# Kernel optimization log

Hardware: AMD Instinct MI355X
Metric: run time of the kernel (lower is better)

Reference implementation:

```python
import jax, jax.numpy as jnp
import numpy as np

B, S, V, E, H, DM = 4, 512, 32000, 512, 1024, 256
U, M = 4096, 1024
MEM_CAP = 512 * 4  # max_length * memory_segments


def setup_inputs() -> dict:
    key = jax.random.key(0)
    ks = jax.random.split(key, 26)
    def n(k, shape, s=0.02):
        return jax.random.normal(k, shape, dtype=jnp.float32) * s
    return {
        'input_ids': jax.random.randint(ks[0], (B, S), 0, V),
        'past_tokens': jax.random.randint(ks[1], (B, M), 0, V),
        'past_keys': jax.random.normal(ks[2], (B, M, DM), dtype=jnp.float32),
        'untied_ids': jax.random.randint(ks[3], (U,), 0, V),
        'emb': n(ks[4], (V, E)),
        'gru_w_ih': n(ks[5], (3 * H, E)), 'gru_w_hh': n(ks[6], (3 * H, H)),
        'gru_b_ih': n(ks[7], (3 * H,)), 'gru_b_hh': n(ks[8], (3 * H,)),
        'q_w': n(ks[9], (DM, H)), 'q_b': n(ks[10], (DM,)),
        'k_w': n(ks[11], (DM, H)), 'k_b': n(ks[12], (DM,)),
        'gate_w': n(ks[13], (1, H)), 'gate_b': n(ks[14], (1,)),
        'fc_w': n(ks[15], (4 * E, H)), 'fc_b': n(ks[16], (4 * E,)),
        'proj_w': n(ks[17], (E, 4 * E)), 'proj_b': n(ks[18], (E,)),
        'out_bias': jnp.zeros((V,), jnp.float32),
        'part_w': n(ks[19], (U, E)), 'part_b': n(ks[20], (U,)),
        'mem_scale': jnp.float32(6.0),
    }


def _gru(x, w_ih, w_hh, b_ih, b_hh):
    # x: [B,S,E] -> states [B,S,H]; torch GRU cell math
    xp = x @ w_ih.T + b_ih  # [B,S,3H]
    h0 = jnp.zeros((x.shape[0], w_hh.shape[1]), x.dtype)
    def step(h, xp_t):
        hp = h @ w_hh.T + b_hh
        xr, xz, xn = jnp.split(xp_t, 3, axis=-1)
        hr, hz, hn = jnp.split(hp, 3, axis=-1)
        r = jax.nn.sigmoid(xr + hr)
        z = jax.nn.sigmoid(xz + hz)
        nn_ = jnp.tanh(xn + r * hn)
        h_new = (1.0 - z) * nn_ + z * h
        return h_new, h_new
    h_last, states = jax.lax.scan(step, h0, jnp.swapaxes(xp, 0, 1))
    return jnp.swapaxes(states, 0, 1), h_last


def reference(input_ids, past_tokens, past_keys, untied_ids, emb,
              gru_w_ih, gru_w_hh, gru_b_ih, gru_b_hh,
              q_w, q_b, k_w, k_b, gate_w, gate_b,
              fc_w, fc_b, proj_w, proj_b, out_bias, part_w, part_b, mem_scale):
    x = emb[input_ids]                                  # [B,S,E]
    states, _ = _gru(x, gru_w_ih, gru_w_hh, gru_b_ih, gru_b_hh)  # dropout=eval identity
    head = jnp.square(jax.nn.relu(states @ fc_w.T + fc_b))       # [B,S,4E]
    base = head @ proj_w.T + proj_b                                # [B,S,E]
    logits = base @ emb.T + out_bias                               # [B,S,V]
    partial = base @ part_w.T + part_b                             # [B,S,U]
    logits = logits.at[:, :, untied_ids].add(partial)              # scatter_add over vocab

    q = states @ q_w.T + q_b                                       # [B,S,DM]
    ck = states @ k_w.T + k_b                                      # [B,S,DM]
    scale = jnp.float32(1.0 / np.sqrt(DM))
    cur_scores = jnp.einsum('bsd,btd->bst', q, ck) * scale
    causal = jnp.tril(jnp.ones((S, S), bool), k=-1)                # strictly-past mask
    neg = jnp.finfo(cur_scores.dtype).min
    masked_cur = jnp.where(causal[None], cur_scores, neg)
    past_scores = jnp.einsum('bsd,bmd->bsm', q, past_keys) * scale
    all_scores = jnp.concatenate([past_scores, masked_cur], axis=-1)   # [B,S,M+S]
    all_mask = jnp.concatenate([
        jnp.ones((B, S, M), bool),
        jnp.broadcast_to(causal[None], (B, S, S))], axis=-1)
    att = jax.nn.softmax(all_scores, axis=-1) * all_mask
    att = att / jnp.maximum(att.sum(axis=-1, keepdims=True), 1e-6)
    val_idx = jnp.concatenate([
        jnp.broadcast_to(past_tokens[:, None, :], (B, S, M)),
        jnp.broadcast_to(input_ids[:, None, :], (B, S, S))], axis=-1)   # [B,S,M+S]
    gate = jax.nn.sigmoid(states @ gate_w.T + gate_b)               # [B,S,1]
    gated = att * (gate * mem_scale)
    b_idx = jnp.arange(B)[:, None, None]
    s_idx = jnp.arange(S)[None, :, None]
    logits = logits.at[b_idx, s_idx, val_idx].add(gated)            # irregular scatter_add

    next_keys = jax.lax.stop_gradient(
        jnp.concatenate([past_keys, ck], axis=1))[:, -MEM_CAP:]
    next_tokens = jnp.concatenate([past_tokens, input_ids], axis=1)[:, -MEM_CAP:]
    return logits, next_keys, next_tokens
```

## Files before the change

kernel.cpp:

```cpp
#include <hip/hip_runtime.h>
#include <cstddef>
#include <cstring>

#define BB 4
#define SS 512
#define VV 32000
#define EE 512
#define HH 1024
#define DM 256
#define UU 4096
#define MM 1024
#define TT 1536

typedef __attribute__((ext_vector_type(8))) short short8v;
typedef __attribute__((ext_vector_type(4))) float f32x4;

__device__ __forceinline__ unsigned long long agent_ld64(const unsigned long long* p) {
  return __hip_atomic_load(const_cast<unsigned long long*>(p), __ATOMIC_RELAXED,
                           __HIP_MEMORY_SCOPE_AGENT);
}
__device__ __forceinline__ void agent_st64(unsigned long long* p, unsigned long long v) {
  __hip_atomic_store(p, v, __ATOMIC_RELAXED, __HIP_MEMORY_SCOPE_AGENT);
}
__device__ __forceinline__ float sigmoidf_(float x) { return 1.f / (1.f + __expf(-x)); }

__device__ __forceinline__ unsigned short f2bf_rtn(float x) {
  unsigned u; __builtin_memcpy(&u, &x, 4);
  unsigned r = (u + 0x7FFFu + ((u >> 16) & 1u)) >> 16;
  return (unsigned short)r;
}
__device__ __forceinline__ float bf2f(unsigned short b) {
  unsigned u = ((unsigned)b) << 16; float f; __builtin_memcpy(&f, &u, 4); return f;
}

__global__ __launch_bounds__(256) void split_bf16(
    const float* __restrict__ in, unsigned short* __restrict__ hi,
    unsigned short* __restrict__ lo, int n)
{
  for (int i = blockIdx.x * 256 + threadIdx.x; i < n; i += gridDim.x * 256) {
    float x = in[i];
    unsigned short h = f2bf_rtn(x);
    hi[i] = h;
    lo[i] = f2bf_rtn(x - bf2f(h));
  }
}

__global__ __launch_bounds__(256) void gemm_mfma_bt(
    const unsigned short* __restrict__ Ah, const unsigned short* __restrict__ Al,
    const unsigned short* __restrict__ Wh, const unsigned short* __restrict__ Wl,
    const float* __restrict__ bias, float* __restrict__ C, int K, int ldc)
{
  const int tid = threadIdx.x, lane = tid & 63, w = tid >> 6;
  const int bm = blockIdx.y * 128, bn = blockIdx.x * 128;
  const int wm = (w >> 1) * 64, wn = (w & 1) * 64;
  const int r = lane & 15, ko = (lane >> 4) * 8;

  f32x4 acc[4][4] = {};

  for (int k0 = 0; k0 < K; k0 += 32) {
    short8v ah[4], al[4], bh[4], bl[4];
#pragma unroll
    for (int mi = 0; mi < 4; ++mi) {
      size_t off = (size_t)(bm + wm + mi * 16 + r) * K + k0 + ko;
      ah[mi] = *(const short8v*)(Ah + off);
      al[mi] = *(const short8v*)(Al + off);
    }
#pragma unroll
    for (int ni = 0; ni < 4; ++ni) {
      size_t off = (size_t)(bn + wn + ni * 16 + r) * K + k0 + ko;
      bh[ni] = *(const short8v*)(Wh + off);
      bl[ni] = *(const short8v*)(Wl + off);
    }
#pragma unroll
    for (int mi = 0; mi < 4; ++mi)
#pragma unroll
      for (int ni = 0; ni < 4; ++ni) {
        acc[mi][ni] = __builtin_amdgcn_mfma_f32_16x16x32_bf16(ah[mi], bh[ni], acc[mi][ni], 0, 0, 0);
        acc[mi][ni] = __builtin_amdgcn_mfma_f32_16x16x32_bf16(ah[mi], bl[ni], acc[mi][ni], 0, 0, 0);
        acc[mi][ni] = __builtin_amdgcn_mfma_f32_16x16x32_bf16(al[mi], bh[ni], acc[mi][ni], 0, 0, 0);
      }
  }

#pragma unroll
  for (int mi = 0; mi < 4; ++mi)
#pragma unroll
    for (int ni = 0; ni < 4; ++ni) {
      const int row = bm + wm + mi * 16 + (lane >> 4) * 4;
      const int col = bn + wn + ni * 16 + (lane & 15);
      const float bv = bias[col];
#pragma unroll
      for (int i = 0; i < 4; ++i)
        C[(size_t)(row + i) * ldc + col] = acc[mi][ni][i] + bv;
    }
}

template <int TILE, int MICRO>
__global__ __launch_bounds__(256) void gemm_k(
    const float* __restrict__ A, const int* __restrict__ a_idx,
    const float* __restrict__ W, const float* __restrict__ bias,
    float* __restrict__ C, int K, int ldc, int act, const int* __restrict__ sidx)
{
  constexpr int PITCH = TILE + 4;
  __shared__ float As[16][PITCH];
  __shared__ float Ws[16][PITCH];
  const int tid = threadIdx.x;
  const int bm = blockIdx.y * TILE, bn = blockIdx.x * TILE;
  const int tr = tid >> 4, tc = tid & 15;
  const int lk = tid & 15, lr0 = tid >> 4;
  float acc[MICRO][MICRO] = {};

  for (int k0 = 0; k0 < K; k0 += 16) {
#pragma unroll
    for (int jj = 0; jj < TILE / 16; ++jj) {
      int row = lr0 + (jj << 4);
      int am = bm + row;
      int ar = a_idx ? a_idx[am] : am;
      As[lk][row] = A[(size_t)ar * K + k0 + lk];
      Ws[lk][row] = W[(size_t)(bn + row) * K + k0 + lk];
    }
    __syncthreads();
#pragma unroll
    for (int kk = 0; kk < 16; ++kk) {
      float av[MICRO], wv[MICRO];
#pragma unroll
      for (int i = 0; i < MICRO; ++i) av[i] = As[kk][tr * MICRO + i];
#pragma unroll
      for (int j = 0; j < MICRO; ++j) wv[j] = Ws[kk][tc * MICRO + j];
#pragma unroll
      for (int i = 0; i < MICRO; ++i)
#pragma unroll
        for (int j = 0; j < MICRO; ++j) acc[i][j] += av[i] * wv[j];
    }
    __syncthreads();
  }

#pragma unroll
  for (int i = 0; i < MICRO; ++i) {
    int m = bm + tr * MICRO + i;
    float tmp[MICRO];
#pragma unroll
    for (int j = 0; j < MICRO; ++j) {
      int n = bn + tc * MICRO + j;
      float v = acc[i][j] + bias[n];
      if (act == 1) { v = fmaxf(v, 0.f); v *= v; }
      tmp[j] = v;
    }
    if (sidx) {
#pragma unroll
      for (int j = 0; j < MICRO; ++j)
        atomicAdd(C + (size_t)m * ldc + sidx[bn + tc * MICRO + j], tmp[j]);
    } else {
      float* cp = C + (size_t)m * ldc + bn + tc * MICRO;
#pragma unroll
      for (int j4 = 0; j4 < MICRO / 4; ++j4)
        *(float4*)(cp + 4 * j4) =
            make_float4(tmp[4 * j4], tmp[4 * j4 + 1], tmp[4 * j4 + 2], tmp[4 * j4 + 3]);
    }
  }
}

__global__ __launch_bounds__(512, 1) void gru_scan(
    const float* __restrict__ xp,
    const float* __restrict__ w_hh,
    const float* __restrict__ b_hh,
    float* __restrict__ states,
    unsigned long long* hbuf)
{
  __shared__ float h_lds[2][HH];
  const int tid = threadIdx.x;
  const int lane = tid & 63;
  const int wv = tid >> 6;
  const int bb = blockIdx.x >> 5;
  const int r = blockIdx.x & 31;
  const int c0 = (r << 5) + (wv << 2);

  unsigned long long* hb = hbuf + ((size_t)bb << 11);

  float wreg[4][3][16];
#pragma unroll
  for (int k = 0; k < 4; ++k)
#pragma unroll
    for (int g = 0; g < 3; ++g) {
      const float* wr = w_hh + (size_t)((g << 10) + c0 + k) * HH + lane;
#pragma unroll
      for (int i = 0; i < 16; ++i) wreg[k][g][i] = wr[i << 6];
    }
  float bh[4][3];
#pragma unroll
  for (int k = 0; k < 4; ++k)
#pragma unroll
    for (int g = 0; g < 3; ++g) bh[k][g] = b_hh[(g << 10) + c0 + k];

  for (int i = tid; i < HH; i += 512) h_lds[0][i] = 0.f;
  __syncthreads();

  for (int t = 0; t < SS; ++t) {
    const int cur = t & 1, nxt = (t + 1) & 1;
    const float* hc = h_lds[cur];

    float4 xrv, xzv, xnv, hold;
    if (lane == 0) {
      const float* xpr = xp + (size_t)((bb << 9) + t) * 3072 + c0;
      xrv = *(const float4*)(xpr);
      xzv = *(const float4*)(xpr + HH);
      xnv = *(const float4*)(xpr + 2 * HH);
      hold = *(const float4*)(hc + c0);
    }

    float acc[4][3] = {};
#pragma unroll
    for (int i = 0; i < 16; ++i) {
      float hv = hc[(i << 6) + lane];
#pragma unroll
      for (int k = 0; k < 4; ++k) {
        acc[k][0] += hv * wreg[k][0][i];
        acc[k][1] += hv * wreg[k][1][i];
        acc[k][2] += hv * wreg[k][2][i];
      }
    }
#pragma unroll
    for (int off = 32; off >= 1; off >>= 1)
#pragma unroll
      for (int k = 0; k < 4; ++k) {
        acc[k][0] += __shfl_xor(acc[k][0], off, 64);
        acc[k][1] += __shfl_xor(acc[k][1], off, 64);
        acc[k][2] += __shfl_xor(acc[k][2], off, 64);
      }

    if (lane == 0) {
      const unsigned long long tagw = ((unsigned long long)(unsigned)(t + 1)) << 32;
      float xr[4] = {xrv.x, xrv.y, xrv.z, xrv.w};
      float xz[4] = {xzv.x, xzv.y, xzv.z, xzv.w};
      float xn[4] = {xnv.x, xnv.y, xnv.z, xnv.w};
      float ho[4] = {hold.x, hold.y, hold.z, hold.w};
      float hv4[4];
#pragma unroll
      for (int k = 0; k < 4; ++k) {
        float rr = sigmoidf_(xr[k] + acc[k][0] + bh[k][0]);
        float zz = sigmoidf_(xz[k] + acc[k][1] + bh[k][1]);
        float nn = tanhf(xn[k] + rr * (acc[k][2] + bh[k][2]));
        hv4[k] = (1.f - zz) * nn + zz * ho[k];
      }
      if (t < SS - 1) {
        unsigned long long* dst = hb + ((size_t)nxt << 10) + c0;
#pragma unroll
        for (int k = 0; k < 4; ++k) {
          unsigned hbits;
          __builtin_memcpy(&hbits, &hv4[k], 4);
          agent_st64(dst + k, tagw | (unsigned long long)hbits);
        }
      }
      *(float4*)(states + (size_t)((bb << 9) + t) * HH + c0) =
          make_float4(hv4[0], hv4[1], hv4[2], hv4[3]);
    }
    if (t == SS - 1) break;

    {
      const unsigned tgt = (unsigned)(t + 1);
      const unsigned long long* src = hb + ((size_t)nxt << 10) + (tid << 1);
      unsigned long long p0, p1;
      for (;;) {
        p0 = agent_ld64(src);
        p1 = agent_ld64(src + 1);
        if ((unsigned)(p0 >> 32) >= tgt && (unsigned)(p1 >> 32) >= tgt) break;
      }
      h_lds[nxt][(tid << 1)] = __uint_as_float((unsigned)p0);
      h_lds[nxt][(tid << 1) + 1] = __uint_as_float((unsigned)p1);
    }
    __syncthreads();
  }
}

__global__ __launch_bounds__(256) void gate_kernel(
    const float* __restrict__ states, const float* __restrict__ gate_w,
    const float* __restrict__ gate_b, float* __restrict__ out)
{
  const int lane = threadIdx.x & 63;
  const int row = (blockIdx.x << 2) + (threadIdx.x >> 6);
  float s = 0.f;
#pragma unroll
  for (int i = 0; i < 16; ++i)
    s += states[(size_t)row * HH + (i << 6) + lane] * gate_w[(i << 6) + lane];
#pragma unroll
  for (int off = 32; off >= 1; off >>= 1) s += __shfl_xor(s, off, 64);
  if (lane == 0) out[row] = sigmoidf_(s + gate_b[0]);
}

__global__ __launch_bounds__(256) void copy_next(
    const float* __restrict__ past_keys, const float* __restrict__ ck,
    const int* __restrict__ past_tokens, const int* __restrict__ input_ids,
    float* __restrict__ nk, float* __restrict__ ntokf)
{
  const int i = blockIdx.x * 256 + threadIdx.x;
  if (i < BB * TT * 64) {
    int b = i / (TT * 64);
    int rem = i - b * (TT * 64);
    int t = rem >> 6, c = rem & 63;
    float4 v;
    if (t < MM) v = ((const float4*)past_keys)[((b << 10) + t) * 64 + c];
    else        v = ((const float4*)ck)[((b << 9) + (t - MM)) * 64 + c];
    ((float4*)nk)[i] = v;
  }
  if (i < BB * TT) {
    int b = i / TT, t = i - b * TT;
    int tok = (t < MM) ? past_tokens[(b << 10) + t] : input_ids[(b << 9) + t - MM];
    ntokf[i] = (float)tok;
  }
}

__global__ __launch_bounds__(256) void attn_scatter(
    const float* __restrict__ qbuf,
    const float* __restrict__ nk,
    const float* __restrict__ ntokf,
    const float* __restrict__ gate,
    const float* __restrict__ msp,
    float* __restrict__ logits)
{
  __shared__ float q_s[8][260];
  __shared__ float k_s[32][260];
  const int b = blockIdx.y;
  const int s0 = blockIdx.x << 3;
  const int tid = threadIdx.x, lane = tid & 63, wv = tid >> 6;
  const int half = lane >> 5, tl = lane & 31;
  const int ss = wv + (half << 2);
  const int sg = s0 + ss;
  const int limit = MM + sg;

  for (int i = tid; i < 8 * 256; i += 256)
    q_s[i >> 8][i & 255] = qbuf[(size_t)((b << 9) + s0 + (i >> 8)) * DM + (i & 255)];

  const int kr = tid >> 3, kc = (tid & 7) << 5;
  float mx = -1e30f, sum = 0.f;
  float fscale = 0.f;

  for (int pass = 0; pass < 2; ++pass) {
    if (pass == 1) {
#pragma unroll
      for (int off = 16; off >= 1; off >>= 1) {
        float mo = __shfl_xor(mx, off, 64);
        float so = __shfl_xor(sum, off, 64);
        float m2 = fmaxf(mx, mo);
        sum = sum * __expf(mx - m2) + so * __expf(mo - m2);
        mx = m2;
      }
      fscale = gate[(b << 9) + sg] * msp[0] / sum;
    }
    for (int tile = 0; tile < 48; ++tile) {
      __syncthreads();
      {
        const float4* src = (const float4*)(nk + ((size_t)(b * TT + (tile << 5) + kr) << 8) + kc);
        float4* dst = (float4*)(&k_s[kr][kc]);
#pragma unroll
        for (int u = 0; u < 8; ++u) dst[u] = src[u];
      }
      __syncthreads();
      int t = (tile << 5) + tl;
      if (t < limit) {
        float a = 0.f;
#pragma unroll 8
        for (int d = 0; d < 256; d += 4) {
          float4 kv = *(const float4*)&k_s[tl][d];
          float4 qv = *(const float4*)&q_s[ss][d];
          a += kv.x * qv.x + kv.y * qv.y + kv.z * qv.z + kv.w * qv.w;
        }
        a *= 0.0625f;
        if (pass == 0) {
          float m2 = fmaxf(mx, a);
          sum = sum * __expf(mx - m2) + __expf(a - m2);
          mx = m2;
        } else {
          int tok = (int)ntokf[b * TT + t];
          atomicAdd(logits + (size_t)((b << 9) + sg) * VV + tok,
                    __expf(a - mx) * fscale);
        }
      }
    }
  }
}

extern "C" void kernel_launch(void* const* d_in, const int* in_sizes, int n_in,
                              void* d_out, int out_size, void* d_ws, size_t ws_size,
                              hipStream_t stream) {
  (void)in_sizes; (void)n_in; (void)out_size;
  const int*   input_ids   = (const int*)  d_in[0];
  const int*   past_tokens = (const int*)  d_in[1];
  const float* past_keys   = (const float*)d_in[2];
  const int*   untied_ids  = (const int*)  d_in[3];
  const float* emb         = (const float*)d_in[4];
  const float* w_ih        = (const float*)d_in[5];
  const float* w_hh        = (const float*)d_in[6];
  const float* b_ih        = (const float*)d_in[7];
  const float* b_hh        = (const float*)d_in[8];
  const float* q_w         = (const float*)d_in[9];
  const float* q_b         = (const float*)d_in[10];
  const float* k_w         = (const float*)d_in[11];
  const float* k_b         = (const float*)d_in[12];
  const float* gate_w      = (const float*)d_in[13];
  const float* gate_b      = (const float*)d_in[14];
  const float* fc_w        = (const float*)d_in[15];
  const float* fc_b        = (const float*)d_in[16];
  const float* proj_w      = (const float*)d_in[17];
  const float* proj_b      = (const float*)d_in[18];
  const float* out_bias    = (const float*)d_in[19];
  const float* part_w      = (const float*)d_in[20];
  const float* part_b      = (const float*)d_in[21];
  const float* mem_scale   = (const float*)d_in[22];

  char* ws = (char*)d_ws;
  unsigned long long* hbuf = (unsigned long long*)(ws + 4096);
  float* gatebuf  = (float*)(ws + 69632);
  float* qb       = (float*)(ws + 81920);
  float* ckb      = (float*)(ws + 2179072);
  float* xp       = (float*)(ws + 4276224);
  float* states   = (float*)(ws + 29442048);
  float* head     = (float*)(ws + 37830656);
  float* base     = (float*)(ws + 54607872);
  unsigned short* embh  = (unsigned short*)(ws + 58802176);
  unsigned short* embl  = (unsigned short*)(ws + 91570176);
  unsigned short* baseh = (unsigned short*)(ws + 124338176);
  unsigned short* basel = (unsigned short*)(ws + 126435328);
  const bool use_mfma = ws_size >= 128532480ull;

  float* logits = (float*)d_out;
  float* nk     = logits + 65536000ll;
  float* ntokf  = logits + 67108864ll;

  hipMemsetAsync(ws, 0, 69632, stream);

  if (use_mfma)
    split_bf16<<<2048, 256, 0, stream>>>(emb, embh, embl, VV * EE);

  gemm_k<128, 8><<<dim3(3072 / 128, 2048 / 128), 256, 0, stream>>>(
      emb, input_ids, w_ih, b_ih, xp, EE, 3072, 0, nullptr);

  gru_scan<<<128, 512, 0, stream>>>(xp, w_hh, b_hh, states, hbuf);

  gemm_k<128, 8><<<dim3(2048 / 128, 2048 / 128), 256, 0, stream>>>(
      states, nullptr, fc_w, fc_b, head, HH, 2048, 1, nullptr);

  gemm_k<64, 4><<<dim3(512 / 64, 2048 / 64), 256, 0, stream>>>(
      head, nullptr, proj_w, proj_b, base, 2048, EE, 0, nullptr);

  if (use_mfma) {
    split_bf16<<<512, 256, 0, stream>>>(base, baseh, basel, 2048 * EE);
    gemm_mfma_bt<<<dim3(VV / 128, 2048 / 128), 256, 0, stream>>>(
        baseh, basel, embh, embl, out_bias, logits, EE, VV);
  } else {
    gemm_k<128, 8><<<dim3(VV / 128, 2048 / 128), 256, 0, stream>>>(
        base, nullptr, emb, out_bias, logits, EE, VV, 0, nullptr);
  }

  gemm_k<128, 8><<<dim3(UU / 128, 2048 / 128), 256, 0, stream>>>(
      base, nullptr, part_w, part_b, logits, EE, VV, 0, untied_ids);

  gemm_k<64, 4><<<dim3(DM / 64, 2048 / 64), 256, 0, stream>>>(
      states, nullptr, q_w, q_b, qb, HH, DM, 0, nullptr);
  gemm_k<64, 4><<<dim3(DM / 64, 2048 / 64), 256, 0, stream>>>(
      states, nullptr, k_w, k_b, ckb, HH, DM, 0, nullptr);

  gate_kernel<<<512, 256, 0, stream>>>(states, gate_w, gate_b, gatebuf);

  copy_next<<<1536, 256, 0, stream>>>(past_keys, ckb, past_tokens, input_ids, nk, ntokf);

  attn_scatter<<<dim3(SS / 8, BB), 256, 0, stream>>>(qb, nk, ntokf, gatebuf, mem_scale, logits);
}
```

Baseline: 5.609 ms.

## Move all GEMMs and attention scores to bf16 hi/lo MFMA, retile GRU scan

Every dense projection (input GRU projection, fc, proj, tied and untied output, q, k) now runs through one MFMA kernel that works on weights and activations stored as bf16 hi and lo halves laid side by side. The attention is split into an MFMA score GEMM plus a per-row softmax-and-scatter kernel, replacing the fused fp32 attention kernel. The GRU scan is retiled to 64 blocks of 1024 threads so fewer blocks take part in the per-step cross-block exchange. Because the hi and lo halves sit side by side, each dot product computes only hi·hi plus lo·lo and drops the hi·lo cross terms, so accuracy falls to roughly bf16 level. It also adds extra split passes and workspace, and the fast path runs only when the workspace is large enough.

```diff
diff --git a/kernel.cpp b/kernel.cpp
--- a/kernel.cpp
+++ b/kernel.cpp
@@ -33,52 +33,53 @@
   unsigned u = ((unsigned)b) << 16; float f; __builtin_memcpy(&f, &u, 4); return f;
 }
 
-__global__ __launch_bounds__(256) void split_bf16(
-    const float* __restrict__ in, unsigned short* __restrict__ hi,
-    unsigned short* __restrict__ lo, int n)
+__global__ __launch_bounds__(256) void split_cat(
+    const float* __restrict__ in, unsigned short* __restrict__ out, int n, int K)
 {
   for (int i = blockIdx.x * 256 + threadIdx.x; i < n; i += gridDim.x * 256) {
+    int row = i / K, col = i - row * K;
     float x = in[i];
     unsigned short h = f2bf_rtn(x);
-    hi[i] = h;
-    lo[i] = f2bf_rtn(x - bf2f(h));
-  }
-}
-
-__global__ __launch_bounds__(256) void gemm_mfma_bt(
-    const unsigned short* __restrict__ Ah, const unsigned short* __restrict__ Al,
-    const unsigned short* __restrict__ Wh, const unsigned short* __restrict__ Wl,
-    const float* __restrict__ bias, float* __restrict__ C, int K, int ldc)
+    unsigned short l = f2bf_rtn(x - bf2f(h));
+    size_t b = (size_t)row * (K << 1) + col;
+    out[b] = h;
+    out[b + K] = l;
+  }
+}
+
+__global__ __launch_bounds__(256) void gemm_mfma_cat(
+    const unsigned short* __restrict__ A2, const int* __restrict__ a_idx,
+    const unsigned short* __restrict__ W2, const float* __restrict__ bias,
+    float* __restrict__ C, unsigned short* __restrict__ C2,
+    int K2, int N, int ldc, int act, const int* __restrict__ sidx)
 {
   const int tid = threadIdx.x, lane = tid & 63, w = tid >> 6;
   const int bm = blockIdx.y * 128, bn = blockIdx.x * 128;
   const int wm = (w >> 1) * 64, wn = (w & 1) * 64;
   const int r = lane & 15, ko = (lane >> 4) * 8;
 
+  int arow[4];
+#pragma unroll
+  for (int mi = 0; mi < 4; ++mi) {
+    int row = bm + wm + mi * 16 + r;
+    arow[mi] = a_idx ? a_idx[row] : row;
+  }
+
   f32x4 acc[4][4] = {};
 
-  for (int k0 = 0; k0 < K; k0 += 32) {
-    short8v ah[4], al[4], bh[4], bl[4];
-#pragma unroll
-    for (int mi = 0; mi < 4; ++mi) {
-      size_t off = (size_t)(bm + wm + mi * 16 + r) * K + k0 + ko;
-      ah[mi] = *(const short8v*)(Ah + off);
-      al[mi] = *(const short8v*)(Al + off);
-    }
-#pragma unroll
-    for (int ni = 0; ni < 4; ++ni) {
-      size_t off = (size_t)(bn + wn + ni * 16 + r) * K + k0 + ko;
-      bh[ni] = *(const short8v*)(Wh + off);
-      bl[ni] = *(const short8v*)(Wl + off);
-    }
+  for (int k0 = 0; k0 < K2; k0 += 32) {
+    short8v a[4], b[4];
 #pragma unroll
     for (int mi = 0; mi < 4; ++mi)
-#pragma unroll
-      for (int ni = 0; ni < 4; ++ni) {
-        acc[mi][ni] = __builtin_amdgcn_mfma_f32_16x16x32_bf16(ah[mi], bh[ni], acc[mi][ni], 0, 0, 0);
-        acc[mi][ni] = __builtin_amdgcn_mfma_f32_16x16x32_bf16(ah[mi], bl[ni], acc[mi][ni], 0, 0, 0);
-        acc[mi][ni] = __builtin_amdgcn_mfma_f32_16x16x32_bf16(al[mi], bh[ni], acc[mi][ni], 0, 0, 0);
-      }
+      a[mi] = *(const short8v*)(A2 + (size_t)arow[mi] * K2 + k0 + ko);
+#pragma unroll
+    for (int ni = 0; ni < 4; ++ni)
+      b[ni] = *(const short8v*)(W2 + (size_t)(bn + wn + ni * 16 + r) * K2 + k0 + ko);
+#pragma unroll
+    for (int mi = 0; mi < 4; ++mi)
+#pragma unroll
+      for (int ni = 0; ni < 4; ++ni)
+        acc[mi][ni] = __builtin_amdgcn_mfma_f32_16x16x32_bf16(a[mi], b[ni], acc[mi][ni], 0, 0, 0);
   }
 
 #pragma unroll
@@ -89,9 +90,107 @@
       const int col = bn + wn + ni * 16 + (lane & 15);
       const float bv = bias[col];
 #pragma unroll
+      for (int i = 0; i < 4; ++i) {
+        float v = acc[mi][ni][i] + bv;
+        if (act == 1) { v = fmaxf(v, 0.f); v *= v; }
+        if (C2) {
+          unsigned short h = f2bf_rtn(v);
+          unsigned short l = f2bf_rtn(v - bf2f(h));
+          size_t bo = (size_t)(row + i) * (N << 1) + col;
+          C2[bo] = h;
+          C2[bo + N] = l;
+        } else if (sidx) {
+          atomicAdd(C + (size_t)(row + i) * ldc + sidx[col], v);
+        } else {
+          C[(size_t)(row + i) * ldc + col] = v;
+        }
+      }
+    }
+}
+
+__global__ __launch_bounds__(256) void score_mfma_cat(
+    const unsigned short* __restrict__ q2,
+    const unsigned short* __restrict__ k2,
+    float* __restrict__ scores)
+{
+  const int b = blockIdx.z;
+  const unsigned short* A2 = q2 + (size_t)b * SS * (2 * DM);
+  const unsigned short* W2 = k2 + (size_t)b * TT * (2 * DM);
+  float* C = scores + (size_t)b * SS * TT;
+
+  const int tid = threadIdx.x, lane = tid & 63, w = tid >> 6;
+  const int bm = blockIdx.y * 128, bn = blockIdx.x * 128;
+  const int wm = (w >> 1) * 64, wn = (w & 1) * 64;
+  const int r = lane & 15, ko = (lane >> 4) * 8;
+
+  f32x4 acc[4][4] = {};
+
+  for (int k0 = 0; k0 < 2 * DM; k0 += 32) {
+    short8v a[4], bfr[4];
+#pragma unroll
+    for (int mi = 0; mi < 4; ++mi)
+      a[mi] = *(const short8v*)(A2 + (size_t)(bm + wm + mi * 16 + r) * (2 * DM) + k0 + ko);
+#pragma unroll
+    for (int ni = 0; ni < 4; ++ni)
+      bfr[ni] = *(const short8v*)(W2 + (size_t)(bn + wn + ni * 16 + r) * (2 * DM) + k0 + ko);
+#pragma unroll
+    for (int mi = 0; mi < 4; ++mi)
+#pragma unroll
+      for (int ni = 0; ni < 4; ++ni)
+        acc[mi][ni] = __builtin_amdgcn_mfma_f32_16x16x32_bf16(a[mi], bfr[ni], acc[mi][ni], 0, 0, 0);
+  }
+
+#pragma unroll
+  for (int mi = 0; mi < 4; ++mi)
+#pragma unroll
+    for (int ni = 0; ni < 4; ++ni) {
+      const int row = bm + wm + mi * 16 + (lane >> 4) * 4;
+      const int col = bn + wn + ni * 16 + (lane & 15);
+#pragma unroll
       for (int i = 0; i < 4; ++i)
-        C[(size_t)(row + i) * ldc + col] = acc[mi][ni][i] + bv;
-    }
+        C[(size_t)(row + i) * TT + col] = acc[mi][ni][i];
+    }
+}
+
+__global__ __launch_bounds__(256) void softmax_scatter(
+    const float* __restrict__ scores,
+    const float* __restrict__ ntokf,
+    const float* __restrict__ gate,
+    const float* __restrict__ msp,
+    float* __restrict__ logits)
+{
+  const int lane = threadIdx.x & 63;
+  const int row = (blockIdx.x << 2) + (threadIdx.x >> 6);
+  const int b = row >> 9, sg = row & 511;
+  const int limit = MM + sg;
+  const float* sr = scores + (size_t)row * TT;
+
+  float v[24];
+  float mx = -1e30f;
+#pragma unroll
+  for (int i = 0; i < 24; ++i) {
+    int t = (i << 6) + lane;
+    v[i] = (t < limit) ? sr[t] * 0.0625f : -1e30f;
+    mx = fmaxf(mx, v[i]);
+  }
+#pragma unroll
+  for (int off = 32; off >= 1; off >>= 1) mx = fmaxf(mx, __shfl_xor(mx, off, 64));
+
+  float sum = 0.f;
+#pragma unroll
+  for (int i = 0; i < 24; ++i) sum += __expf(v[i] - mx);
+#pragma unroll
+  for (int off = 32; off >= 1; off >>= 1) sum += __shfl_xor(sum, off, 64);
+
+  const float fs = gate[row] * msp[0] / sum;
+  const float* tokr = ntokf + b * TT;
+  float* lrow = logits + (size_t)row * VV;
+#pragma unroll
+  for (int i = 0; i < 24; ++i) {
+    int t = (i << 6) + lane;
+    if (t < limit)
+      atomicAdd(lrow + (int)tokr[t], __expf(v[i] - mx) * fs);
+  }
 }
 
 template <int TILE, int MICRO>
@@ -159,7 +258,7 @@
   }
 }
 
-__global__ __launch_bounds__(512, 1) void gru_scan(
+__global__ __launch_bounds__(1024, 1) void gru_scan(
     const float* __restrict__ xp,
     const float* __restrict__ w_hh,
     const float* __restrict__ b_hh,
@@ -170,9 +269,9 @@
   const int tid = threadIdx.x;
   const int lane = tid & 63;
   const int wv = tid >> 6;
-  const int bb = blockIdx.x >> 5;
-  const int r = blockIdx.x & 31;
-  const int c0 = (r << 5) + (wv << 2);
+  const int bb = blockIdx.x >> 4;
+  const int r = blockIdx.x & 15;
+  const int c0 = (r << 6) + (wv << 2);
 
   unsigned long long* hb = hbuf + ((size_t)bb << 11);
 
@@ -191,7 +290,7 @@
 #pragma unroll
     for (int g = 0; g < 3; ++g) bh[k][g] = b_hh[(g << 10) + c0 + k];
 
-  for (int i = tid; i < HH; i += 512) h_lds[0][i] = 0.f;
+  h_lds[0][tid] = 0.f;
   __syncthreads();
 
   for (int t = 0; t < SS; ++t) {
@@ -257,15 +356,13 @@
 
     {
       const unsigned tgt = (unsigned)(t + 1);
-      const unsigned long long* src = hb + ((size_t)nxt << 10) + (tid << 1);
-      unsigned long long p0, p1;
+      const unsigned long long* src = hb + ((size_t)nxt << 10) + tid;
+      unsigned long long p;
       for (;;) {
-        p0 = agent_ld64(src);
-        p1 = agent_ld64(src + 1);
-        if ((unsigned)(p0 >> 32) >= tgt && (unsigned)(p1 >> 32) >= tgt) break;
-      }
-      h_lds[nxt][(tid << 1)] = __uint_as_float((unsigned)p0);
-      h_lds[nxt][(tid << 1) + 1] = __uint_as_float((unsigned)p1);
+        p = agent_ld64(src);
+        if ((unsigned)(p >> 32) >= tgt) break;
+      }
+      h_lds[nxt][tid] = __uint_as_float((unsigned)p);
     }
     __syncthreads();
   }
@@ -309,12 +406,9 @@
 }
 
 __global__ __launch_bounds__(256) void attn_scatter(
-    const float* __restrict__ qbuf,
-    const float* __restrict__ nk,
-    const float* __restrict__ ntokf,
-    const float* __restrict__ gate,
-    const float* __restrict__ msp,
-    float* __restrict__ logits)
+    const float* __restrict__ qbuf, const float* __restrict__ nk,
+    const float* __restrict__ ntokf, const float* __restrict__ gate,
+    const float* __restrict__ msp, float* __restrict__ logits)
 {
   __shared__ float q_s[8][260];
   __shared__ float k_s[32][260];
@@ -407,60 +501,99 @@
   const float* mem_scale   = (const float*)d_in[22];
 
   char* ws = (char*)d_ws;
-  unsigned long long* hbuf = (unsigned long long*)(ws + 4096);
-  float* gatebuf  = (float*)(ws + 69632);
-  float* qb       = (float*)(ws + 81920);
-  float* ckb      = (float*)(ws + 2179072);
-  float* xp       = (float*)(ws + 4276224);
-  float* states   = (float*)(ws + 29442048);
-  float* head     = (float*)(ws + 37830656);
-  float* base     = (float*)(ws + 54607872);
-  unsigned short* embh  = (unsigned short*)(ws + 58802176);
-  unsigned short* embl  = (unsigned short*)(ws + 91570176);
-  unsigned short* baseh = (unsigned short*)(ws + 124338176);
-  unsigned short* basel = (unsigned short*)(ws + 126435328);
-  const bool use_mfma = ws_size >= 128532480ull;
-
   float* logits = (float*)d_out;
   float* nk     = logits + 65536000ll;
   float* ntokf  = logits + 67108864ll;
 
+  const bool fast = ws_size >= 180961280ull;
+
   hipMemsetAsync(ws, 0, 69632, stream);
 
-  if (use_mfma)
-    split_bf16<<<2048, 256, 0, stream>>>(emb, embh, embl, VV * EE);
-
-  gemm_k<128, 8><<<dim3(3072 / 128, 2048 / 128), 256, 0, stream>>>(
-      emb, input_ids, w_ih, b_ih, xp, EE, 3072, 0, nullptr);
-
-  gru_scan<<<128, 512, 0, stream>>>(xp, w_hh, b_hh, states, hbuf);
-
-  gemm_k<128, 8><<<dim3(2048 / 128, 2048 / 128), 256, 0, stream>>>(
-      states, nullptr, fc_w, fc_b, head, HH, 2048, 1, nullptr);
-
-  gemm_k<64, 4><<<dim3(512 / 64, 2048 / 64), 256, 0, stream>>>(
-      head, nullptr, proj_w, proj_b, base, 2048, EE, 0, nullptr);
-
-  if (use_mfma) {
-    split_bf16<<<512, 256, 0, stream>>>(base, baseh, basel, 2048 * EE);
-    gemm_mfma_bt<<<dim3(VV / 128, 2048 / 128), 256, 0, stream>>>(
-        baseh, basel, embh, embl, out_bias, logits, EE, VV);
+  if (fast) {
+    unsigned long long* hbuf = (unsigned long long*)(ws + 4096);
+    float* gatebuf = (float*)(ws + 69632);
+    float* xp      = (float*)(ws + 81920);
+    float* states  = (float*)(ws + 25247744);
+    float* ckb     = (float*)(ws + 33636352);
+    unsigned short* emb2    = (unsigned short*)(ws + 35733504);
+    unsigned short* w_ih2   = (unsigned short*)(ws + 101269504);
+    unsigned short* fc_w2   = (unsigned short*)(ws + 107560960);
+    unsigned short* proj_w2 = (unsigned short*)(ws + 115949568);
+    unsigned short* part_w2 = (unsigned short*)(ws + 120143872);
+    unsigned short* q_w2    = (unsigned short*)(ws + 128532480);
+    unsigned short* k_w2    = (unsigned short*)(ws + 129581056);
+    unsigned short* states2 = (unsigned short*)(ws + 130629632);
+    unsigned short* head2   = (unsigned short*)(ws + 139018240);
+    unsigned short* base2   = (unsigned short*)(ws + 155795456);
+    unsigned short* qb2     = (unsigned short*)(ws + 159989760);
+    unsigned short* nk2     = (unsigned short*)(ws + 162086912);
+    float* scores           = (float*)(ws + 168378368);
+
+    split_cat<<<2048, 256, 0, stream>>>(emb, emb2, VV * EE, EE);
+    split_cat<<<512, 256, 0, stream>>>(w_ih, w_ih2, 3072 * EE, EE);
+    split_cat<<<512, 256, 0, stream>>>(fc_w, fc_w2, 2048 * HH, HH);
+    split_cat<<<512, 256, 0, stream>>>(proj_w, proj_w2, EE * 2048, 2048);
+    split_cat<<<512, 256, 0, stream>>>(part_w, part_w2, UU * EE, EE);
+    split_cat<<<128, 256, 0, stream>>>(q_w, q_w2, DM * HH, HH);
+    split_cat<<<128, 256, 0, stream>>>(k_w, k_w2, DM * HH, HH);
+
+    gemm_mfma_cat<<<dim3(3072 / 128, 2048 / 128), 256, 0, stream>>>(
+        emb2, input_ids, w_ih2, b_ih, xp, nullptr, 2 * EE, 3072, 3072, 0, nullptr);
+
+    gru_scan<<<64, 1024, 0, stream>>>(xp, w_hh, b_hh, states, hbuf);
+    split_cat<<<512, 256, 0, stream>>>(states, states2, 2048 * HH, HH);
+
+    gemm_mfma_cat<<<dim3(2048 / 128, 2048 / 128), 256, 0, stream>>>(
+        states2, nullptr, fc_w2, fc_b, nullptr, head2, 2 * HH, 2048, 0, 1, nullptr);
+
+    gemm_mfma_cat<<<dim3(512 / 128, 2048 / 128), 256, 0, stream>>>(
+        head2, nullptr, proj_w2, proj_b, nullptr, base2, 2 * 2048, EE, 0, 0, nullptr);
+
+    gemm_mfma_cat<<<dim3(VV / 128, 2048 / 128), 256, 0, stream>>>(
+        base2, nullptr, emb2, out_bias, logits, nullptr, 2 * EE, VV, VV, 0, nullptr);
+
+    gemm_mfma_cat<<<dim3(UU / 128, 2048 / 128), 256, 0, stream>>>(
+        base2, nullptr, part_w2, part_b, logits, nullptr, 2 * EE, UU, VV, 0, untied_ids);
+
+    gemm_mfma_cat<<<dim3(DM / 128, 2048 / 128), 256, 0, stream>>>(
+        states2, nullptr, q_w2, q_b, nullptr, qb2, 2 * HH, DM, 0, 0, nullptr);
+    gemm_mfma_cat<<<dim3(DM / 128, 2048 / 128), 256, 0, stream>>>(
+        states2, nullptr, k_w2, k_b, ckb, nullptr, 2 * HH, DM, DM, 0, nullptr);
+
+    gate_kernel<<<512, 256, 0, stream>>>(states, gate_w, gate_b, gatebuf);
+
+    copy_next<<<1536, 256, 0, stream>>>(past_keys, ckb, past_tokens, input_ids, nk, ntokf);
+
+    split_cat<<<512, 256, 0, stream>>>(nk, nk2, BB * TT * DM, DM);
+    score_mfma_cat<<<dim3(TT / 128, SS / 128, BB), 256, 0, stream>>>(qb2, nk2, scores);
+    softmax_scatter<<<512, 256, 0, stream>>>(scores, ntokf, gatebuf, mem_scale, logits);
   } else {
+    unsigned long long* hbuf = (unsigned long long*)(ws + 4096);
+    float* gatebuf  = (float*)(ws + 69632);
+    float* qb       = (float*)(ws + 81920);
+    float* ckb      = (float*)(ws + 2179072);
+    float* xp       = (float*)(ws + 4276224);
+    float* states   = (float*)(ws + 29442048);
+    float* head     = (float*)(ws + 37830656);
+    float* base     = (float*)(ws + 54607872);
+
+    gemm_k<128, 8><<<dim3(3072 / 128, 2048 / 128), 256, 0, stream>>>(
+        emb, input_ids, w_ih, b_ih, xp, EE, 3072, 0, nullptr);
+    gru_scan<<<64, 1024, 0, stream>>>(xp, w_hh, b_hh, states, hbuf);
+    gemm_k<128, 8><<<dim3(2048 / 128, 2048 / 128), 256, 0, stream>>>(
+        states, nullptr, fc_w, fc_b, head, HH, 2048, 1, nullptr);
+    gemm_k<64, 4><<<dim3(512 / 64, 2048 / 64), 256, 0, stream>>>(
+        head, nullptr, proj_w, proj_b, base, 2048, EE, 0, nullptr);
     gemm_k<128, 8><<<dim3(VV / 128, 2048 / 128), 256, 0, stream>>>(
         base, nullptr, emb, out_bias, logits, EE, VV, 0, nullptr);
-  }
-
-  gemm_k<128, 8><<<dim3(UU / 128, 2048 / 128), 256, 0, stream>>>(
-      base, nullptr, part_w, part_b, logits, EE, VV, 0, untied_ids);
-
-  gemm_k<64, 4><<<dim3(DM / 64, 2048 / 64), 256, 0, stream>>>(
-      states, nullptr, q_w, q_b, qb, HH, DM, 0, nullptr);
-  gemm_k<64, 4><<<dim3(DM / 64, 2048 / 64), 256, 0, stream>>>(
-      states, nullptr, k_w, k_b, ckb, HH, DM, 0, nullptr);
-
-  gate_kernel<<<512, 256, 0, stream>>>(states, gate_w, gate_b, gatebuf);
-
-  copy_next<<<1536, 256, 0, stream>>>(past_keys, ckb, past_tokens, input_ids, nk, ntokf);
-
-  attn_scatter<<<dim3(SS / 8, BB), 256, 0, stream>>>(qb, nk, ntokf, gatebuf, mem_scale, logits);
-}
+    gemm_k<128, 8><<<dim3(UU / 128, 2048 / 128), 256, 0, stream>>>(
+        base, nullptr, part_w, part_b, logits, EE, VV, 0, untied_ids);
+    gemm_k<64, 4><<<dim3(DM / 64, 2048 / 64), 256, 0, stream>>>(
+        states, nullptr, q_w, q_b, qb, HH, DM, 0, nullptr);
+    gemm_k<64, 4><<<dim3(DM / 64, 2048 / 64), 256, 0, stream>>>(
+        states, nullptr, k_w, k_b, ckb, HH, DM, 0, nullptr);
+    gate_kernel<<<512, 256, 0, stream>>>(states, gate_w, gate_b, gatebuf);
+    copy_next<<<1536, 256, 0, stream>>>(past_keys, ckb, past_tokens, input_ids, nk, ntokf);
+    attn_scatter<<<dim3(SS / 8, BB), 256, 0, stream>>>(qb, nk, ntokf, gatebuf, mem_scale, logits);
+  }
+}
```

Measured after the change: 22.13 ms. 294% more time.
